# Optimization experiments

Hardware: AMD Instinct MI355X
Metric: run time of the kernel (lower is better)

Reference implementation:

```python
import jax, jax.numpy as jnp
import numpy as np

B, N, C, H = 4, 1024, 1024, 16
D = C // H  # head_dim = 64


def setup_inputs() -> dict:
    key = jax.random.key(0)
    k1, k2, k3 = jax.random.split(key, 3)
    x = jax.random.normal(k1, (B, N, C), dtype=jnp.float32)
    Wqkv = jax.random.normal(k2, (3 * C, C), dtype=jnp.float32) * (C ** -0.5)
    Wproj = jax.random.normal(k3, (C, C), dtype=jnp.float32) * (C ** -0.5)
    bproj = jnp.zeros((C,), dtype=jnp.float32)
    epoch = 25  # selects mask_2 (window w=8) per the original branching
    return {"x": x, "Wqkv": Wqkv, "Wproj": Wproj, "bproj": bproj, "epoch": epoch}


def _band_mask(n, w):
    # get_attn_mask(N, w) == (|i - j| <= w) for every row (boundary cases included)
    idx = jnp.arange(n)
    return jnp.abs(idx[:, None] - idx[None, :]) <= w


def reference(x, Wqkv, Wproj, bproj, epoch):
    b, n, c = x.shape
    d = c // H
    # qkv linear (no bias), then the module's per-head interleaved split:
    # view(B,N,H,3d) -> permute(B,H,N,3d) -> tensor_split into q,k,v
    qkv = jnp.einsum('bnc,oc->bno', x, Wqkv)            # [B,N,3C]
    qkv = qkv.reshape(b, n, H, 3 * d).transpose(0, 2, 1, 3)  # [B,H,N,3d]
    q, k, v = jnp.split(qkv, 3, axis=-1)                # each [B,H,N,d]
    scale = d ** -0.5
    score = jnp.einsum('bhid,bhjd->bhij', q, k) * scale  # [B,H,N,N]
    if epoch is not None and epoch < 50:
        if epoch < 20:
            w = 6
        elif epoch < 30:
            w = 8
        elif epoch < 40:
            w = 10
        else:
            w = 12
        mask = _band_mask(n, w)  # [N,N] bool
        score = jnp.where(mask[None, None], score, jnp.float32(-1e9))
    attn = jax.nn.softmax(score, axis=-1)
    ctx = jnp.einsum('bhij,bhjd->bhid', attn, v)         # [B,H,N,d]
    ctx = ctx.transpose(0, 2, 1, 3).reshape(b, n, c)     # [B,N,C]
    out = jnp.einsum('bnc,oc->bno', ctx, Wproj) + bproj
    return out
```

## Files before the change

### kernel.cpp

```cpp
#include <hip/hip_runtime.h>
#include <hip/hip_bf16.h>


typedef __bf16 bf16x8_t __attribute__((ext_vector_type(8)));
typedef unsigned short u16x8_t __attribute__((ext_vector_type(8)));
typedef float f32x4_t __attribute__((ext_vector_type(4)));

__device__ __forceinline__ void load_lds16(const void* g, void* l) {
    __builtin_amdgcn_global_load_lds(
        (__attribute__((address_space(1))) void*)(g),
        (__attribute__((address_space(3))) void*)(l),
        16, 0, 0);
}

__global__ __launch_bounds__(256) void convert_all(
    const float* __restrict__ x, const float* __restrict__ wqkv,
    const float* __restrict__ wproj,
    __hip_bfloat16* __restrict__ xb, __hip_bfloat16* __restrict__ wqkvb,
    __hip_bfloat16* __restrict__ wprojb)
{
    const size_t t = (size_t)blockIdx.x * 256 + threadIdx.x;
    size_t i = t * 8;
    const float* src;
    __hip_bfloat16* dst;
    if (i < 4194304) {
        src = x; dst = xb;
    } else if (i < 4194304 + 3145728) {
        src = wqkv; dst = wqkvb; i -= 4194304;
    } else {
        src = wproj; dst = wprojb; i -= 4194304 + 3145728;
    }
    float4 v0 = *reinterpret_cast<const float4*>(src + i);
    float4 v1 = *reinterpret_cast<const float4*>(src + i + 4);
    union { u16x8_t v; __hip_bfloat16 h[8]; } u;
    u.h[0] = __float2bfloat16(v0.x); u.h[1] = __float2bfloat16(v0.y);
    u.h[2] = __float2bfloat16(v0.z); u.h[3] = __float2bfloat16(v0.w);
    u.h[4] = __float2bfloat16(v1.x); u.h[5] = __float2bfloat16(v1.y);
    u.h[6] = __float2bfloat16(v1.z); u.h[7] = __float2bfloat16(v1.w);
    *reinterpret_cast<u16x8_t*>(dst + i) = u.v;
}

__global__ __launch_bounds__(512, 2) void gemm1_qkv256(
    const __hip_bfloat16* __restrict__ A,
    const __hip_bfloat16* __restrict__ B,
    __hip_bfloat16* __restrict__ C)
{
    __shared__ __align__(16) char smem[114688];
    const int tid = threadIdx.x;

    const int orig = blockIdx.y * 16 + blockIdx.x;
    const int xcd = orig & 7, slot = orig >> 3;
    const int hi = slot >> 4;
    const int s  = xcd * 2 + hi;
    const int w  = slot & 15;
    const int m0 = ((s & 3) * 4 + (w & 3)) * 256;
    const int n0 = ((s >> 2) * 4 + (w >> 2)) * 192;

    const int wave = tid >> 6, lane = tid & 63;
    const int wr = wave >> 2, wc = wave & 3;
    const int lr = lane & 15, kg = lane >> 4;
    const int K = 1024, Nn = 3072;

    const int qa0 = tid, qa1 = tid + 512;
    const int qb0 = tid, qb1 = tid + 256;
    const int ra0 = qa0 >> 2, sa0 = ((qa0 & 3) ^ ((ra0 >> 1) & 3)) * 16;
    const int ra1 = qa1 >> 2, sa1 = ((qa1 & 3) ^ ((ra1 >> 1) & 3)) * 16;
    const int rb0 = qb0 >> 2, sb0 = ((qb0 & 3) ^ ((rb0 >> 1) & 3)) * 16;
    const int rb1 = qb1 >> 2, sb1 = ((qb1 & 3) ^ ((rb1 >> 1) & 3)) * 16;
    const char* Asrc0 = (const char*)(A + (size_t)(m0 + ra0) * K) + sa0;
    const char* Asrc1 = (const char*)(A + (size_t)(m0 + ra1) * K) + sa1;
    const char* Bsrc0 = (const char*)(B + (size_t)(n0 + rb0) * K) + sb0;
    const char* Bsrc1 = (const char*)(B + (size_t)(n0 + rb1) * K) + sb1;
    const bool bextra = (tid >= 256);

#define STAGE_A(t) { const int sb_ = ((t) & 3) * 28672; const int ko_ = (t) * 64; \
    load_lds16(Asrc0 + ko_, smem + sb_ + qa0 * 16);                                \
    load_lds16(Asrc1 + ko_, smem + sb_ + qa1 * 16); }
#define STAGE_B(t) { const int sb_ = ((t) & 3) * 28672; const int ko_ = (t) * 64; \
    load_lds16(Bsrc0 + ko_, smem + sb_ + 16384 + qb0 * 16);                        \
    if (bextra) load_lds16(Bsrc1 + ko_, smem + sb_ + 16384 + qb1 * 16); }

    f32x4_t acc[8][3] = {};
    const int rsw = ((kg ^ ((lr >> 1) & 3)) * 16);
    const int arow = wr * 128 + lr;
    const int brow = wc * 48 + lr;

    STAGE_A(0); STAGE_B(0);
    STAGE_A(1); STAGE_B(1);
    if (!bextra) { asm volatile("s_waitcnt vmcnt(4)" ::: "memory"); }
    else         { asm volatile("s_waitcnt vmcnt(3)" ::: "memory"); }
    __builtin_amdgcn_s_barrier();

    for (int t = 0; t < 32; ++t) {
        const int sb_ = (t & 3) * 28672;
        bf16x8_t a_[8], b_[3];
#pragma unroll
        for (int mi = 0; mi < 4; ++mi)
            a_[mi] = *(const bf16x8_t*)(smem + sb_ + (arow + mi * 16) * 64 + rsw);
#pragma unroll
        for (int ni = 0; ni < 3; ++ni)
            b_[ni] = *(const bf16x8_t*)(smem + sb_ + 16384 + (brow + ni * 16) * 64 + rsw);
        if (t < 30) STAGE_A(t + 2);
        __builtin_amdgcn_s_barrier();
        __builtin_amdgcn_s_setprio(1);
#pragma unroll
        for (int mi = 0; mi < 4; ++mi)
#pragma unroll
            for (int ni = 0; ni < 3; ++ni)
                acc[mi][ni] = __builtin_amdgcn_mfma_f32_16x16x32_bf16(
                    a_[mi], b_[ni], acc[mi][ni], 0, 0, 0);
        __builtin_amdgcn_s_setprio(0);
        __builtin_amdgcn_s_barrier();
#pragma unroll
        for (int mi = 4; mi < 8; ++mi)
            a_[mi] = *(const bf16x8_t*)(smem + sb_ + (arow + mi * 16) * 64 + rsw);
        if (t < 30) {
            STAGE_B(t + 2);
            if (!bextra) { asm volatile("s_waitcnt vmcnt(4)" ::: "memory"); }
            else         { asm volatile("s_waitcnt vmcnt(3)" ::: "memory"); }
        } else {
            asm volatile("s_waitcnt vmcnt(0)" ::: "memory");
        }
        __builtin_amdgcn_s_barrier();
        __builtin_amdgcn_s_setprio(1);
#pragma unroll
        for (int mi = 4; mi < 8; ++mi)
#pragma unroll
            for (int ni = 0; ni < 3; ++ni)
                acc[mi][ni] = __builtin_amdgcn_mfma_f32_16x16x32_bf16(
                    a_[mi], b_[ni], acc[mi][ni], 0, 0, 0);
        __builtin_amdgcn_s_setprio(0);
        __builtin_amdgcn_s_barrier();
    }
#undef STAGE_A
#undef STAGE_B

    __syncthreads();
    __hip_bfloat16* cl = (__hip_bfloat16*)smem;
#pragma unroll
    for (int mi = 0; mi < 8; ++mi)
#pragma unroll
        for (int ni = 0; ni < 3; ++ni)
#pragma unroll
            for (int r = 0; r < 4; ++r)
                cl[(wr * 128 + mi * 16 + kg * 4 + r) * 200 + wc * 48 + ni * 16 + lr] =
                    __float2bfloat16(acc[mi][ni][r]);
    __syncthreads();
#pragma unroll
    for (int c = 0; c < 12; ++c) {
        const int id = tid + c * 512;
        const int row = id / 24, cc = id - row * 24;
        f32x4_t v = *(const f32x4_t*)(smem + row * 400 + cc * 16);
        *(f32x4_t*)((char*)C + ((size_t)(m0 + row) * Nn + n0) * 2 + cc * 16) = v;
    }
}

__global__ __launch_bounds__(512, 2) void gemm2_proj128(
    const __hip_bfloat16* __restrict__ A,
    const __hip_bfloat16* __restrict__ B,
    float* __restrict__ C,
    const float* __restrict__ bias)
{
    __shared__ __align__(16) char smem[65536];
    const int tid = threadIdx.x;
    const int orig = blockIdx.y * 8 + blockIdx.x;
    const int wgid = (orig & 7) * 32 + (orig >> 3);
    const int m0 = (wgid >> 3) * 128, n0 = (wgid & 7) * 128;

    const int wave = tid >> 6, lane = tid & 63;
    const int wr = wave >> 2, wc = wave & 3;
    const int lr = lane & 15, kg = lane >> 4;
    const int K = 1024, Nn = 1024;

    const int q = tid;
    const int row = q >> 2, sl = ((q & 3) ^ ((row >> 1) & 3)) * 16;
    const char* Asrc = (const char*)(A + (size_t)(m0 + row) * K) + sl;
    const char* Bsrc = (const char*)(B + (size_t)(n0 + row) * K) + sl;

#define STAGE2(t) { const int sb_ = ((t) & 3) * 16384; const int ko_ = (t) * 64; \
    load_lds16(Asrc + ko_, smem + sb_ + q * 16);                                  \
    load_lds16(Bsrc + ko_, smem + sb_ + 8192 + q * 16); }

    f32x4_t acc[4][2] = {};
    const int rsw = ((kg ^ ((lr >> 1) & 3)) * 16);
    const int arow = wr * 64 + lr;
    const int brow = wc * 32 + lr;

    STAGE2(0); STAGE2(1);
    asm volatile("s_waitcnt vmcnt(2)" ::: "memory");
    __builtin_amdgcn_s_barrier();

    for (int t = 0; t < 32; ++t) {
        const int sb_ = (t & 3) * 16384;
        if (t < 30) {
            STAGE2(t + 2);
            asm volatile("s_waitcnt vmcnt(4)" ::: "memory");
        } else if (t == 30) {
            asm volatile("s_waitcnt vmcnt(2)" ::: "memory");
        } else {
            asm volatile("s_waitcnt vmcnt(0)" ::: "memory");
        }
        __builtin_amdgcn_s_barrier();
        bf16x8_t a_[4], b_[2];
#pragma unroll
        for (int mi = 0; mi < 4; ++mi)
            a_[mi] = *(const bf16x8_t*)(smem + sb_ + (arow + mi * 16) * 64 + rsw);
#pragma unroll
        for (int ni = 0; ni < 2; ++ni)
            b_[ni] = *(const bf16x8_t*)(smem + sb_ + 8192 + (brow + ni * 16) * 64 + rsw);
        __builtin_amdgcn_s_setprio(1);
#pragma unroll
        for (int mi = 0; mi < 4; ++mi)
#pragma unroll
            for (int ni = 0; ni < 2; ++ni)
                acc[mi][ni] = __builtin_amdgcn_mfma_f32_16x16x32_bf16(
                    a_[mi], b_[ni], acc[mi][ni], 0, 0, 0);
        __builtin_amdgcn_s_setprio(0);
        __builtin_amdgcn_s_barrier();
    }
#undef STAGE2

    __syncthreads();
    float* cf = (float*)smem;
#pragma unroll
    for (int p = 0; p < 2; ++p) {
        if (p) __syncthreads();
        if (wr == p) {
#pragma unroll
            for (int mi = 0; mi < 4; ++mi)
#pragma unroll
                for (int ni = 0; ni < 2; ++ni) {
                    const int scol = wc * 32 + ni * 16 + lr;
#pragma unroll
                    for (int r = 0; r < 4; ++r)
                        cf[(mi * 16 + kg * 4 + r) * 132 + scol] = acc[mi][ni][r];
                }
        }
        __syncthreads();
#pragma unroll
        for (int cc = 0; cc < 4; ++cc) {
            const int chunk = tid + cc * 512;
            const int srow = chunk >> 5;
            const int sc = (chunk & 31) * 4;
            f32x4_t v = *(const f32x4_t*)(smem + srow * 528 + sc * 4);
            const f32x4_t bv = *(const f32x4_t*)(bias + n0 + sc);
            v += bv;
            *(f32x4_t*)(C + (size_t)(m0 + p * 64 + srow) * Nn + n0 + sc) = v;
        }
    }
}

__global__ __launch_bounds__(256) void attn_band_mfma(
    const __hip_bfloat16* __restrict__ qkv,
    __hip_bfloat16* __restrict__ ctx,
    const int* __restrict__ epoch_ptr)
{
    __shared__ __align__(16) __hip_bfloat16 K_lds[128 * 64];
    __shared__ __align__(16) __hip_bfloat16 V_lds[64 * 136];
    __shared__ __hip_bfloat16 P_lds[4][16 * 40];

    const int tid = threadIdx.x;
    const int wave = tid >> 6, lane = tid & 63;
    const int lr = lane & 15, kg = lane >> 4;

    const int bid = blockIdx.x;
    const int tg = bid & 15;
    const int bh = bid >> 4;
    const int h = bh & 15, b = bh >> 4;
    const int base = tg * 64;
    const int i0 = base + wave * 16;

    const int e = *epoch_ptr;
    int w;
    if      (e < 20) w = 6;
    else if (e < 30) w = 8;
    else if (e < 40) w = 10;
    else if (e < 50) w = 12;
    else             w = 1023;

    const size_t rowb = (size_t)b * 1024;
    const int hq = h * 192;

#pragma unroll
    for (int it = 0; it < 4; ++it) {
        const int q = tid + it * 256;
        const int row = q >> 3, s = q & 7;
        const int c = s ^ (row & 7);
        int gk = base - 32 + row;
        gk = gk < 0 ? 0 : (gk > 1023 ? 1023 : gk);
        load_lds16(qkv + (rowb + gk) * 3072 + hq + 64 + c * 8,
                   (char*)K_lds + q * 16);
    }
    {
        const int pr = tid & 63, dg = tid >> 6;
        int gk0 = base - 32 + 2 * pr, gk1 = gk0 + 1;
        gk0 = gk0 < 0 ? 0 : (gk0 > 1023 ? 1023 : gk0);
        gk1 = gk1 < 0 ? 0 : (gk1 > 1023 ? 1023 : gk1);
        const __hip_bfloat16* v0 = qkv + (rowb + gk0) * 3072 + hq + 128 + dg * 16;
        const __hip_bfloat16* v1 = qkv + (rowb + gk1) * 3072 + hq + 128 + dg * 16;
        u16x8_t a0 = *(const u16x8_t*)v0, b0 = *(const u16x8_t*)(v0 + 8);
        u16x8_t a1 = *(const u16x8_t*)v1, b1 = *(const u16x8_t*)(v1 + 8);
#pragma unroll
        for (int c2 = 0; c2 < 8; ++c2) {
            *(unsigned int*)&V_lds[(dg * 16 + c2) * 136 + 2 * pr] =
                (unsigned int)a0[c2] | ((unsigned int)a1[c2] << 16);
            *(unsigned int*)&V_lds[(dg * 16 + 8 + c2) * 136 + 2 * pr] =
                (unsigned int)b0[c2] | ((unsigned int)b1[c2] << 16);
        }
    }

    bf16x8_t aq[2];
#pragma unroll
    for (int ks = 0; ks < 2; ++ks)
        aq[ks] = *(const bf16x8_t*)(qkv + (rowb + i0 + lr) * 3072 + hq + ks * 32 + kg * 8);

    __syncthreads();

    float m[4] = {-1e30f, -1e30f, -1e30f, -1e30f};
    float l[4] = {0.f, 0.f, 0.f, 0.f};
    f32x4_t o[4] = {};

    int jlo = i0 - w;      if (jlo < 0) jlo = 0;
    int jhi = i0 + 15 + w; if (jhi > 1023) jhi = 1023;
    const int t0 = (base >> 5) - 1;

    for (int p = (jlo >> 5); p <= (jhi >> 5); ++p) {
        const int kb = p * 32;
        const int tl = p - t0;

        f32x4_t s2[2] = {};
#pragma unroll
        for (int t = 0; t < 2; ++t)
#pragma unroll
            for (int ks = 0; ks < 2; ++ks) {
                const int lkr = tl * 32 + t * 16 + lr;
                bf16x8_t bk = *(const bf16x8_t*)(
                    (char*)K_lds + lkr * 128 + (((ks * 4 + kg) ^ (lr & 7)) * 16));
                s2[t] = __builtin_amdgcn_mfma_f32_16x16x32_bf16(aq[ks], bk, s2[t], 0, 0, 0);
            }

        float sv[2][4];
#pragma unroll
        for (int t = 0; t < 2; ++t)
#pragma unroll
            for (int r = 0; r < 4; ++r) {
                const int qi = i0 + kg * 4 + r;
                const int j  = kb + t * 16 + lr;
                int d = qi - j; if (d < 0) d = -d;
                sv[t][r] = (d <= w) ? s2[t][r] * 0.125f : -1e30f;
            }

        float tm[4];
#pragma unroll
        for (int r = 0; r < 4; ++r) tm[r] = fmaxf(sv[0][r], sv[1][r]);
#pragma unroll
        for (int msk = 1; msk < 16; msk <<= 1)
#pragma unroll
            for (int r = 0; r < 4; ++r) tm[r] = fmaxf(tm[r], __shfl_xor(tm[r], msk));

        float sc[4], ps[4], pvv[2][4];
#pragma unroll
        for (int r = 0; r < 4; ++r) {
            const float mn = fmaxf(m[r], tm[r]);
            sc[r] = __expf(m[r] - mn);
            pvv[0][r] = __expf(sv[0][r] - mn);
            pvv[1][r] = __expf(sv[1][r] - mn);
            ps[r] = pvv[0][r] + pvv[1][r];
            m[r] = mn;
        }
#pragma unroll
        for (int msk = 1; msk < 16; msk <<= 1)
#pragma unroll
            for (int r = 0; r < 4; ++r) ps[r] += __shfl_xor(ps[r], msk);
#pragma unroll
        for (int r = 0; r < 4; ++r) l[r] = l[r] * sc[r] + ps[r];
#pragma unroll
        for (int ni = 0; ni < 4; ++ni)
#pragma unroll
            for (int r = 0; r < 4; ++r) o[ni][r] *= sc[r];

#pragma unroll
        for (int t = 0; t < 2; ++t)
#pragma unroll
            for (int r = 0; r < 4; ++r)
                P_lds[wave][(kg * 4 + r) * 40 + t * 16 + lr] =
                    __float2bfloat16(pvv[t][r]);

        bf16x8_t ap = *(const bf16x8_t*)&P_lds[wave][lr * 40 + kg * 8];
#pragma unroll
        for (int ni = 0; ni < 4; ++ni) {
            bf16x8_t bv = *(const bf16x8_t*)&V_lds[(ni * 16 + lr) * 136 + tl * 32 + kg * 8];
            o[ni] = __builtin_amdgcn_mfma_f32_16x16x32_bf16(ap, bv, o[ni], 0, 0, 0);
        }
    }

#pragma unroll
    for (int ni = 0; ni < 4; ++ni)
#pragma unroll
        for (int r = 0; r < 4; ++r)
            ctx[(rowb + i0 + kg * 4 + r) * 1024 + h * 64 + ni * 16 + lr] =
                __float2bfloat16(o[ni][r] / l[r]);
}

extern "C" void kernel_launch(void* const* d_in, const int* in_sizes, int n_in,
                              void* d_out, int out_size, void* d_ws, size_t ws_size,
                              hipStream_t stream)
{
    const float* x     = (const float*)d_in[0];
    const float* Wqkv  = (const float*)d_in[1];
    const float* Wproj = (const float*)d_in[2];
    const float* bproj = (const float*)d_in[3];
    const int*   epoch = (const int*)d_in[4];

    char* ws = (char*)d_ws;
    __hip_bfloat16* xb     = (__hip_bfloat16*)(ws);
    __hip_bfloat16* wqkvb  = (__hip_bfloat16*)(ws + 8388608);
    __hip_bfloat16* wprojb = (__hip_bfloat16*)(ws + 8388608 + 6291456);
    __hip_bfloat16* qkvb   = (__hip_bfloat16*)(ws + 16777216);
    __hip_bfloat16* ctxb   = (__hip_bfloat16*)(ws + 16777216 + 25165824);

    convert_all<<<4096, 256, 0, stream>>>(x, Wqkv, Wproj, xb, wqkvb, wprojb);

    gemm1_qkv256<<<dim3(16, 16), 512, 0, stream>>>(xb, wqkvb, qkvb);

    attn_band_mfma<<<1024, 256, 0, stream>>>(qkvb, ctxb, epoch);

    gemm2_proj128<<<dim3(8, 32), 512, 0, stream>>>(
        ctxb, wprojb, (float*)d_out, bproj);
}
```

Measured before the change: 73.93 us.

## Fuse fp32-to-bf16 conversion into GEMM tile staging and drop convert kernel

Removes the separate conversion kernel and has both GEMMs load fp32 inputs into registers, convert to bf16, and store to swizzled LDS, with a register-prefetch pipeline replacing async global-to-LDS loads. This avoids writing and re-reading bf16 copies of x and weights plus one launch. In exchange GEMM1 reads fp32 operands repeatedly across tiles, doubling operand bytes, and loses direct-to-LDS loads, adding register pressure and VALU conversion work in the main loop.

```diff
diff --git a/kernel.cpp b/kernel.cpp
--- a/kernel.cpp
+++ b/kernel.cpp
@@ -13,36 +13,18 @@
         16, 0, 0);
 }
 
-__global__ __launch_bounds__(256) void convert_all(
-    const float* __restrict__ x, const float* __restrict__ wqkv,
-    const float* __restrict__ wproj,
-    __hip_bfloat16* __restrict__ xb, __hip_bfloat16* __restrict__ wqkvb,
-    __hip_bfloat16* __restrict__ wprojb)
-{
-    const size_t t = (size_t)blockIdx.x * 256 + threadIdx.x;
-    size_t i = t * 8;
-    const float* src;
-    __hip_bfloat16* dst;
-    if (i < 4194304) {
-        src = x; dst = xb;
-    } else if (i < 4194304 + 3145728) {
-        src = wqkv; dst = wqkvb; i -= 4194304;
-    } else {
-        src = wproj; dst = wprojb; i -= 4194304 + 3145728;
-    }
-    float4 v0 = *reinterpret_cast<const float4*>(src + i);
-    float4 v1 = *reinterpret_cast<const float4*>(src + i + 4);
-    union { u16x8_t v; __hip_bfloat16 h[8]; } u;
-    u.h[0] = __float2bfloat16(v0.x); u.h[1] = __float2bfloat16(v0.y);
-    u.h[2] = __float2bfloat16(v0.z); u.h[3] = __float2bfloat16(v0.w);
-    u.h[4] = __float2bfloat16(v1.x); u.h[5] = __float2bfloat16(v1.y);
-    u.h[6] = __float2bfloat16(v1.z); u.h[7] = __float2bfloat16(v1.w);
-    *reinterpret_cast<u16x8_t*>(dst + i) = u.v;
-}
-
-__global__ __launch_bounds__(512, 2) void gemm1_qkv256(
-    const __hip_bfloat16* __restrict__ A,
-    const __hip_bfloat16* __restrict__ B,
+__device__ __forceinline__ u16x8_t cvt8(float4 u, float4 v) {
+    union { u16x8_t p; __hip_bfloat16 h[8]; } w;
+    w.h[0] = __float2bfloat16(u.x); w.h[1] = __float2bfloat16(u.y);
+    w.h[2] = __float2bfloat16(u.z); w.h[3] = __float2bfloat16(u.w);
+    w.h[4] = __float2bfloat16(v.x); w.h[5] = __float2bfloat16(v.y);
+    w.h[6] = __float2bfloat16(v.z); w.h[7] = __float2bfloat16(v.w);
+    return w.p;
+}
+
+__global__ __launch_bounds__(512, 2) void gemm1_qkv(
+    const float* __restrict__ A,
+    const float* __restrict__ B,
     __hip_bfloat16* __restrict__ C)
 {
     __shared__ __align__(16) char smem[114688];
@@ -63,79 +45,65 @@
 
     const int qa0 = tid, qa1 = tid + 512;
     const int qb0 = tid, qb1 = tid + 256;
-    const int ra0 = qa0 >> 2, sa0 = ((qa0 & 3) ^ ((ra0 >> 1) & 3)) * 16;
-    const int ra1 = qa1 >> 2, sa1 = ((qa1 & 3) ^ ((ra1 >> 1) & 3)) * 16;
-    const int rb0 = qb0 >> 2, sb0 = ((qb0 & 3) ^ ((rb0 >> 1) & 3)) * 16;
-    const int rb1 = qb1 >> 2, sb1 = ((qb1 & 3) ^ ((rb1 >> 1) & 3)) * 16;
-    const char* Asrc0 = (const char*)(A + (size_t)(m0 + ra0) * K) + sa0;
-    const char* Asrc1 = (const char*)(A + (size_t)(m0 + ra1) * K) + sa1;
-    const char* Bsrc0 = (const char*)(B + (size_t)(n0 + rb0) * K) + sb0;
-    const char* Bsrc1 = (const char*)(B + (size_t)(n0 + rb1) * K) + sb1;
+    const int ra0 = qa0 >> 2, ca0 = ((qa0 & 3) ^ ((ra0 >> 1) & 3)) * 8;
+    const int ra1 = qa1 >> 2, ca1 = ((qa1 & 3) ^ ((ra1 >> 1) & 3)) * 8;
+    const int rb0 = qb0 >> 2, cb0 = ((qb0 & 3) ^ ((rb0 >> 1) & 3)) * 8;
+    const int rb1 = qb1 >> 2, cb1 = ((qb1 & 3) ^ ((rb1 >> 1) & 3)) * 8;
+    const float* Ap0 = A + (size_t)(m0 + ra0) * K + ca0;
+    const float* Ap1 = A + (size_t)(m0 + ra1) * K + ca1;
+    const float* Bp0 = B + (size_t)(n0 + rb0) * K + cb0;
+    const float* Bp1 = B + (size_t)(n0 + rb1) * K + cb1;
     const bool bextra = (tid >= 256);
 
-#define STAGE_A(t) { const int sb_ = ((t) & 3) * 28672; const int ko_ = (t) * 64; \
-    load_lds16(Asrc0 + ko_, smem + sb_ + qa0 * 16);                                \
-    load_lds16(Asrc1 + ko_, smem + sb_ + qa1 * 16); }
-#define STAGE_B(t) { const int sb_ = ((t) & 3) * 28672; const int ko_ = (t) * 64; \
-    load_lds16(Bsrc0 + ko_, smem + sb_ + 16384 + qb0 * 16);                        \
-    if (bextra) load_lds16(Bsrc1 + ko_, smem + sb_ + 16384 + qb1 * 16); }
+    float4 a00 = {}, a01 = {}, a10 = {}, a11 = {};
+    float4 b00 = {}, b01 = {}, b10 = {}, b11 = {};
+
+#define LOADR(t) { const int ko_ = (t) * 32;                                   \
+    a00 = *(const float4*)(Ap0 + ko_); a01 = *(const float4*)(Ap0 + ko_ + 4);  \
+    a10 = *(const float4*)(Ap1 + ko_); a11 = *(const float4*)(Ap1 + ko_ + 4);  \
+    b00 = *(const float4*)(Bp0 + ko_); b01 = *(const float4*)(Bp0 + ko_ + 4);  \
+    if (bextra) { b10 = *(const float4*)(Bp1 + ko_);                           \
+                  b11 = *(const float4*)(Bp1 + ko_ + 4); } }
+#define WRITE(t) { char* d_ = smem + ((t) & 3) * 28672;                        \
+    *(u16x8_t*)(d_ + qa0 * 16) = cvt8(a00, a01);                               \
+    *(u16x8_t*)(d_ + qa1 * 16) = cvt8(a10, a11);                               \
+    *(u16x8_t*)(d_ + 16384 + qb0 * 16) = cvt8(b00, b01);                       \
+    if (bextra) *(u16x8_t*)(d_ + 16384 + qb1 * 16) = cvt8(b10, b11); }
 
     f32x4_t acc[8][3] = {};
     const int rsw = ((kg ^ ((lr >> 1) & 3)) * 16);
     const int arow = wr * 128 + lr;
     const int brow = wc * 48 + lr;
 
-    STAGE_A(0); STAGE_B(0);
-    STAGE_A(1); STAGE_B(1);
-    if (!bextra) { asm volatile("s_waitcnt vmcnt(4)" ::: "memory"); }
-    else         { asm volatile("s_waitcnt vmcnt(3)" ::: "memory"); }
-    __builtin_amdgcn_s_barrier();
+    LOADR(0); WRITE(0);
+    LOADR(1); WRITE(1);
+    LOADR(2);
+    __syncthreads();
 
     for (int t = 0; t < 32; ++t) {
         const int sb_ = (t & 3) * 28672;
         bf16x8_t a_[8], b_[3];
 #pragma unroll
-        for (int mi = 0; mi < 4; ++mi)
+        for (int mi = 0; mi < 8; ++mi)
             a_[mi] = *(const bf16x8_t*)(smem + sb_ + (arow + mi * 16) * 64 + rsw);
 #pragma unroll
         for (int ni = 0; ni < 3; ++ni)
             b_[ni] = *(const bf16x8_t*)(smem + sb_ + 16384 + (brow + ni * 16) * 64 + rsw);
-        if (t < 30) STAGE_A(t + 2);
-        __builtin_amdgcn_s_barrier();
+        if (t < 30) WRITE(t + 2);
+        if (t < 29) LOADR(t + 3);
         __builtin_amdgcn_s_setprio(1);
 #pragma unroll
-        for (int mi = 0; mi < 4; ++mi)
+        for (int mi = 0; mi < 8; ++mi)
 #pragma unroll
             for (int ni = 0; ni < 3; ++ni)
                 acc[mi][ni] = __builtin_amdgcn_mfma_f32_16x16x32_bf16(
                     a_[mi], b_[ni], acc[mi][ni], 0, 0, 0);
         __builtin_amdgcn_s_setprio(0);
-        __builtin_amdgcn_s_barrier();
-#pragma unroll
-        for (int mi = 4; mi < 8; ++mi)
-            a_[mi] = *(const bf16x8_t*)(smem + sb_ + (arow + mi * 16) * 64 + rsw);
-        if (t < 30) {
-            STAGE_B(t + 2);
-            if (!bextra) { asm volatile("s_waitcnt vmcnt(4)" ::: "memory"); }
-            else         { asm volatile("s_waitcnt vmcnt(3)" ::: "memory"); }
-        } else {
-            asm volatile("s_waitcnt vmcnt(0)" ::: "memory");
-        }
-        __builtin_amdgcn_s_barrier();
-        __builtin_amdgcn_s_setprio(1);
-#pragma unroll
-        for (int mi = 4; mi < 8; ++mi)
-#pragma unroll
-            for (int ni = 0; ni < 3; ++ni)
-                acc[mi][ni] = __builtin_amdgcn_mfma_f32_16x16x32_bf16(
-                    a_[mi], b_[ni], acc[mi][ni], 0, 0, 0);
-        __builtin_amdgcn_s_setprio(0);
-        __builtin_amdgcn_s_barrier();
-    }
-#undef STAGE_A
-#undef STAGE_B
-
-    __syncthreads();
+        __syncthreads();
+    }
+#undef LOADR
+#undef WRITE
+
     __hip_bfloat16* cl = (__hip_bfloat16*)smem;
 #pragma unroll
     for (int mi = 0; mi < 8; ++mi)
@@ -155,9 +123,9 @@
     }
 }
 
-__global__ __launch_bounds__(512, 2) void gemm2_proj128(
+__global__ __launch_bounds__(512, 2) void gemm2_proj(
     const __hip_bfloat16* __restrict__ A,
-    const __hip_bfloat16* __restrict__ B,
+    const float* __restrict__ B,
     float* __restrict__ C,
     const float* __restrict__ bias)
 {
@@ -173,34 +141,31 @@
     const int K = 1024, Nn = 1024;
 
     const int q = tid;
-    const int row = q >> 2, sl = ((q & 3) ^ ((row >> 1) & 3)) * 16;
-    const char* Asrc = (const char*)(A + (size_t)(m0 + row) * K) + sl;
-    const char* Bsrc = (const char*)(B + (size_t)(n0 + row) * K) + sl;
-
-#define STAGE2(t) { const int sb_ = ((t) & 3) * 16384; const int ko_ = (t) * 64; \
-    load_lds16(Asrc + ko_, smem + sb_ + q * 16);                                  \
-    load_lds16(Bsrc + ko_, smem + sb_ + 8192 + q * 16); }
+    const int row = q >> 2, cw = ((q & 3) ^ ((row >> 1) & 3)) * 8;
+    const __hip_bfloat16* Ap = A + (size_t)(m0 + row) * K + cw;
+    const float*          Bp = B + (size_t)(n0 + row) * K + cw;
+
+    float4 av = {}, bv0 = {}, bv1 = {};
+
+#define LOADR2(t) { const int ko_ = (t) * 32;                                  \
+    av  = *(const float4*)(Ap + ko_);                        \
+    bv0 = *(const float4*)(Bp + ko_); bv1 = *(const float4*)(Bp + ko_ + 4); }
+#define WRITE2(t) { char* d_ = smem + ((t) & 3) * 16384;                       \
+    *(float4*)(d_ + q * 16) = av;                                              \
+    *(u16x8_t*)(d_ + 8192 + q * 16) = cvt8(bv0, bv1); }
 
     f32x4_t acc[4][2] = {};
     const int rsw = ((kg ^ ((lr >> 1) & 3)) * 16);
     const int arow = wr * 64 + lr;
     const int brow = wc * 32 + lr;
 
-    STAGE2(0); STAGE2(1);
-    asm volatile("s_waitcnt vmcnt(2)" ::: "memory");
-    __builtin_amdgcn_s_barrier();
+    LOADR2(0); WRITE2(0);
+    LOADR2(1); WRITE2(1);
+    LOADR2(2);
+    __syncthreads();
 
     for (int t = 0; t < 32; ++t) {
         const int sb_ = (t & 3) * 16384;
-        if (t < 30) {
-            STAGE2(t + 2);
-            asm volatile("s_waitcnt vmcnt(4)" ::: "memory");
-        } else if (t == 30) {
-            asm volatile("s_waitcnt vmcnt(2)" ::: "memory");
-        } else {
-            asm volatile("s_waitcnt vmcnt(0)" ::: "memory");
-        }
-        __builtin_amdgcn_s_barrier();
         bf16x8_t a_[4], b_[2];
 #pragma unroll
         for (int mi = 0; mi < 4; ++mi)
@@ -208,6 +173,8 @@
 #pragma unroll
         for (int ni = 0; ni < 2; ++ni)
             b_[ni] = *(const bf16x8_t*)(smem + sb_ + 8192 + (brow + ni * 16) * 64 + rsw);
+        if (t < 30) WRITE2(t + 2);
+        if (t < 29) LOADR2(t + 3);
         __builtin_amdgcn_s_setprio(1);
 #pragma unroll
         for (int mi = 0; mi < 4; ++mi)
@@ -216,11 +183,11 @@
                 acc[mi][ni] = __builtin_amdgcn_mfma_f32_16x16x32_bf16(
                     a_[mi], b_[ni], acc[mi][ni], 0, 0, 0);
         __builtin_amdgcn_s_setprio(0);
-        __builtin_amdgcn_s_barrier();
-    }
-#undef STAGE2
-
-    __syncthreads();
+        __syncthreads();
+    }
+#undef LOADR2
+#undef WRITE2
+
     float* cf = (float*)smem;
 #pragma unroll
     for (int p = 0; p < 2; ++p) {
@@ -413,18 +380,13 @@
     const int*   epoch = (const int*)d_in[4];
 
     char* ws = (char*)d_ws;
-    __hip_bfloat16* xb     = (__hip_bfloat16*)(ws);
-    __hip_bfloat16* wqkvb  = (__hip_bfloat16*)(ws + 8388608);
-    __hip_bfloat16* wprojb = (__hip_bfloat16*)(ws + 8388608 + 6291456);
-    __hip_bfloat16* qkvb   = (__hip_bfloat16*)(ws + 16777216);
-    __hip_bfloat16* ctxb   = (__hip_bfloat16*)(ws + 16777216 + 25165824);
-
-    convert_all<<<4096, 256, 0, stream>>>(x, Wqkv, Wproj, xb, wqkvb, wprojb);
-
-    gemm1_qkv256<<<dim3(16, 16), 512, 0, stream>>>(xb, wqkvb, qkvb);
+    __hip_bfloat16* qkvb = (__hip_bfloat16*)(ws);
+    __hip_bfloat16* ctxb = (__hip_bfloat16*)(ws + 25165824);
+
+    gemm1_qkv<<<dim3(16, 16), 512, 0, stream>>>(x, Wqkv, qkvb);
 
     attn_band_mfma<<<1024, 256, 0, stream>>>(qkvb, ctxb, epoch);
 
-    gemm2_proj128<<<dim3(8, 32), 512, 0, stream>>>(
-        ctxb, wprojb, (float*)d_out, bproj);
-}
+    gemm2_proj<<<dim3(8, 32), 512, 0, stream>>>(
+        ctxb, Wproj, (float*)d_out, bproj);
+}
```

New measurement: 68.05 us (median of 2 runs). 1.09x faster.

## Fuse Wproj bf16 conversion into projection GEMM loads and retune gemm1 waitcnts

Applied to the files above, without the earlier changes.

Drops the Wproj conversion from the standalone convert kernel, which now handles only x and Wqkv. The projection GEMM reads fp32 Wproj directly through registers, converts it to bf16 and writes it into LDS, replacing the async global-to-LDS copies with a register-staged, prefetch-ahead pipeline and full __syncthreads. This removes a 4 MB write plus re-read of the bf16 weight copy. In exchange, gemm2 reads twice the B bytes on every tile and loses async LDS loads. The gemm1 vmcnt wait counts for the bextra and non-bextra threads are also swapped.

```diff
diff --git a/kernel.cpp b/kernel.cpp
--- a/kernel.cpp
+++ b/kernel.cpp
@@ -13,11 +13,18 @@
         16, 0, 0);
 }
 
-__global__ __launch_bounds__(256) void convert_all(
+__device__ __forceinline__ u16x8_t cvt8(float4 u, float4 v) {
+    union { u16x8_t p; __hip_bfloat16 h[8]; } w;
+    w.h[0] = __float2bfloat16(u.x); w.h[1] = __float2bfloat16(u.y);
+    w.h[2] = __float2bfloat16(u.z); w.h[3] = __float2bfloat16(u.w);
+    w.h[4] = __float2bfloat16(v.x); w.h[5] = __float2bfloat16(v.y);
+    w.h[6] = __float2bfloat16(v.z); w.h[7] = __float2bfloat16(v.w);
+    return w.p;
+}
+
+__global__ __launch_bounds__(256) void convert_xw(
     const float* __restrict__ x, const float* __restrict__ wqkv,
-    const float* __restrict__ wproj,
-    __hip_bfloat16* __restrict__ xb, __hip_bfloat16* __restrict__ wqkvb,
-    __hip_bfloat16* __restrict__ wprojb)
+    __hip_bfloat16* __restrict__ xb, __hip_bfloat16* __restrict__ wqkvb)
 {
     const size_t t = (size_t)blockIdx.x * 256 + threadIdx.x;
     size_t i = t * 8;
@@ -25,19 +32,12 @@
     __hip_bfloat16* dst;
     if (i < 4194304) {
         src = x; dst = xb;
-    } else if (i < 4194304 + 3145728) {
+    } else {
         src = wqkv; dst = wqkvb; i -= 4194304;
-    } else {
-        src = wproj; dst = wprojb; i -= 4194304 + 3145728;
     }
     float4 v0 = *reinterpret_cast<const float4*>(src + i);
     float4 v1 = *reinterpret_cast<const float4*>(src + i + 4);
-    union { u16x8_t v; __hip_bfloat16 h[8]; } u;
-    u.h[0] = __float2bfloat16(v0.x); u.h[1] = __float2bfloat16(v0.y);
-    u.h[2] = __float2bfloat16(v0.z); u.h[3] = __float2bfloat16(v0.w);
-    u.h[4] = __float2bfloat16(v1.x); u.h[5] = __float2bfloat16(v1.y);
-    u.h[6] = __float2bfloat16(v1.z); u.h[7] = __float2bfloat16(v1.w);
-    *reinterpret_cast<u16x8_t*>(dst + i) = u.v;
+    *reinterpret_cast<u16x8_t*>(dst + i) = cvt8(v0, v1);
 }
 
 __global__ __launch_bounds__(512, 2) void gemm1_qkv256(
@@ -87,8 +87,8 @@
 
     STAGE_A(0); STAGE_B(0);
     STAGE_A(1); STAGE_B(1);
-    if (!bextra) { asm volatile("s_waitcnt vmcnt(4)" ::: "memory"); }
-    else         { asm volatile("s_waitcnt vmcnt(3)" ::: "memory"); }
+    if (!bextra) { asm volatile("s_waitcnt vmcnt(3)" ::: "memory"); }
+    else         { asm volatile("s_waitcnt vmcnt(4)" ::: "memory"); }
     __builtin_amdgcn_s_barrier();
 
     for (int t = 0; t < 32; ++t) {
@@ -116,8 +116,8 @@
             a_[mi] = *(const bf16x8_t*)(smem + sb_ + (arow + mi * 16) * 64 + rsw);
         if (t < 30) {
             STAGE_B(t + 2);
-            if (!bextra) { asm volatile("s_waitcnt vmcnt(4)" ::: "memory"); }
-            else         { asm volatile("s_waitcnt vmcnt(3)" ::: "memory"); }
+            if (!bextra) { asm volatile("s_waitcnt vmcnt(3)" ::: "memory"); }
+            else         { asm volatile("s_waitcnt vmcnt(4)" ::: "memory"); }
         } else {
             asm volatile("s_waitcnt vmcnt(0)" ::: "memory");
         }
@@ -155,9 +155,9 @@
     }
 }
 
-__global__ __launch_bounds__(512, 2) void gemm2_proj128(
+__global__ __launch_bounds__(512, 2) void gemm2_proj(
     const __hip_bfloat16* __restrict__ A,
-    const __hip_bfloat16* __restrict__ B,
+    const float* __restrict__ B,
     float* __restrict__ C,
     const float* __restrict__ bias)
 {
@@ -173,34 +173,31 @@
     const int K = 1024, Nn = 1024;
 
     const int q = tid;
-    const int row = q >> 2, sl = ((q & 3) ^ ((row >> 1) & 3)) * 16;
-    const char* Asrc = (const char*)(A + (size_t)(m0 + row) * K) + sl;
-    const char* Bsrc = (const char*)(B + (size_t)(n0 + row) * K) + sl;
-
-#define STAGE2(t) { const int sb_ = ((t) & 3) * 16384; const int ko_ = (t) * 64; \
-    load_lds16(Asrc + ko_, smem + sb_ + q * 16);                                  \
-    load_lds16(Bsrc + ko_, smem + sb_ + 8192 + q * 16); }
+    const int row = q >> 2, cw = ((q & 3) ^ ((row >> 1) & 3)) * 8;
+    const __hip_bfloat16* Ap = A + (size_t)(m0 + row) * K + cw;
+    const float*          Bp = B + (size_t)(n0 + row) * K + cw;
+
+    float4 av = {}, bv0 = {}, bv1 = {};
+
+#define LOADR2(t) { const int ko_ = (t) * 32;                                  \
+    av  = *(const float4*)(Ap + ko_);                        \
+    bv0 = *(const float4*)(Bp + ko_); bv1 = *(const float4*)(Bp + ko_ + 4); }
+#define WRITE2(t) { char* d_ = smem + ((t) & 3) * 16384;                       \
+    *(float4*)(d_ + q * 16) = av;                                              \
+    *(u16x8_t*)(d_ + 8192 + q * 16) = cvt8(bv0, bv1); }
 
     f32x4_t acc[4][2] = {};
     const int rsw = ((kg ^ ((lr >> 1) & 3)) * 16);
     const int arow = wr * 64 + lr;
     const int brow = wc * 32 + lr;
 
-    STAGE2(0); STAGE2(1);
-    asm volatile("s_waitcnt vmcnt(2)" ::: "memory");
-    __builtin_amdgcn_s_barrier();
+    LOADR2(0); WRITE2(0);
+    LOADR2(1); WRITE2(1);
+    LOADR2(2);
+    __syncthreads();
 
     for (int t = 0; t < 32; ++t) {
         const int sb_ = (t & 3) * 16384;
-        if (t < 30) {
-            STAGE2(t + 2);
-            asm volatile("s_waitcnt vmcnt(4)" ::: "memory");
-        } else if (t == 30) {
-            asm volatile("s_waitcnt vmcnt(2)" ::: "memory");
-        } else {
-            asm volatile("s_waitcnt vmcnt(0)" ::: "memory");
-        }
-        __builtin_amdgcn_s_barrier();
         bf16x8_t a_[4], b_[2];
 #pragma unroll
         for (int mi = 0; mi < 4; ++mi)
@@ -208,6 +205,8 @@
 #pragma unroll
         for (int ni = 0; ni < 2; ++ni)
             b_[ni] = *(const bf16x8_t*)(smem + sb_ + 8192 + (brow + ni * 16) * 64 + rsw);
+        if (t < 30) WRITE2(t + 2);
+        if (t < 29) LOADR2(t + 3);
         __builtin_amdgcn_s_setprio(1);
 #pragma unroll
         for (int mi = 0; mi < 4; ++mi)
@@ -216,11 +215,11 @@
                 acc[mi][ni] = __builtin_amdgcn_mfma_f32_16x16x32_bf16(
                     a_[mi], b_[ni], acc[mi][ni], 0, 0, 0);
         __builtin_amdgcn_s_setprio(0);
-        __builtin_amdgcn_s_barrier();
-    }
-#undef STAGE2
-
-    __syncthreads();
+        __syncthreads();
+    }
+#undef LOADR2
+#undef WRITE2
+
     float* cf = (float*)smem;
 #pragma unroll
     for (int p = 0; p < 2; ++p) {
@@ -413,18 +412,17 @@
     const int*   epoch = (const int*)d_in[4];
 
     char* ws = (char*)d_ws;
-    __hip_bfloat16* xb     = (__hip_bfloat16*)(ws);
-    __hip_bfloat16* wqkvb  = (__hip_bfloat16*)(ws + 8388608);
-    __hip_bfloat16* wprojb = (__hip_bfloat16*)(ws + 8388608 + 6291456);
-    __hip_bfloat16* qkvb   = (__hip_bfloat16*)(ws + 16777216);
-    __hip_bfloat16* ctxb   = (__hip_bfloat16*)(ws + 16777216 + 25165824);
-
-    convert_all<<<4096, 256, 0, stream>>>(x, Wqkv, Wproj, xb, wqkvb, wprojb);
+    __hip_bfloat16* xb    = (__hip_bfloat16*)(ws);
+    __hip_bfloat16* wqkvb = (__hip_bfloat16*)(ws + 8388608);
+    __hip_bfloat16* qkvb  = (__hip_bfloat16*)(ws + 16777216);
+    __hip_bfloat16* ctxb  = (__hip_bfloat16*)(ws + 16777216 + 25165824);
+
+    convert_xw<<<3584, 256, 0, stream>>>(x, Wqkv, xb, wqkvb);
 
     gemm1_qkv256<<<dim3(16, 16), 512, 0, stream>>>(xb, wqkvb, qkvb);
 
     attn_band_mfma<<<1024, 256, 0, stream>>>(qkvb, ctxb, epoch);
 
-    gemm2_proj128<<<dim3(8, 32), 512, 0, stream>>>(
-        ctxb, wprojb, (float*)d_out, bproj);
-}
+    gemm2_proj<<<dim3(8, 32), 512, 0, stream>>>(
+        ctxb, Wproj, (float*)d_out, bproj);
+}
```

Result: faster. 71.55 us (-3.2%).
